# Optimization experiments

Measured on AMD Instinct MI355X. Metric: run time of the kernel, lower is better.

Reference implementation:

```python
import jax, jax.numpy as jnp
import numpy as np

B, SW, SS, D, H = 2, 1024, 256, 1024, 16  # D = hidden_dim*num_heads = 64*16


def _dense_init(key, d_in, d_out):
    # xavier_uniform kernel, zero bias
    lim = np.sqrt(6.0 / (d_in + d_out))
    k = jax.random.uniform(key, (d_in, d_out), jnp.float32, -lim, lim)
    b = jnp.zeros((d_out,), jnp.float32)
    return k, b


def setup_inputs() -> dict:
    key = jax.random.key(0)
    ks = jax.random.split(key, 16)
    inp = {
        'word_inputs': jax.random.normal(ks[0], (B, SW, D), jnp.float32),
        'word_context': jax.random.normal(ks[1], (B, SW, D), jnp.float32),
        'sentence_inputs': jax.random.normal(ks[2], (B, SS, D), jnp.float32),
        'sentence_context': jax.random.normal(ks[3], (B, SS, D), jnp.float32),
        'word_mask': jax.random.uniform(ks[4], (B, H, SW, SW), jnp.float32),
        'sentence_mask': jax.random.uniform(ks[5], (B, H, SS, SS), jnp.float32),
    }
    names = ['wq', 'wk', 'wv', 'wo', 'sq', 'sk', 'sv', 'so']
    for i, n in enumerate(names):
        kk, bb = _dense_init(ks[6 + i], D, D)
        inp[n + '_k'] = kk
        inp[n + '_b'] = bb
    return inp


def _attention(q, k, v, mask):
    # Faithful to source: split heads by raw reshape (B, H, L, hd),
    # scale by sqrt(full key dim), multiplicative mask.
    Bq, Lk, Dm = v.shape[0], v.shape[1], q.shape[-1]
    hd = Dm // H
    qh = jnp.reshape(q, (Bq, H, Lk, hd))
    kh = jnp.reshape(k, (Bq, H, Lk, hd))
    vh = jnp.reshape(v, (Bq, H, Lk, hd))
    scores = jnp.einsum('bhqd,bhkd->bhqk', qh, kh) / jnp.sqrt(jnp.float32(Dm))
    if mask is not None:
        scores = scores * mask
    attn = jax.nn.softmax(scores, axis=-1)
    ctx = jnp.einsum('bhqk,bhkd->bhqd', attn, vh)
    return attn, jnp.reshape(ctx, (Bq, Lk, Dm))


def reference(word_inputs, word_context, sentence_inputs, sentence_context,
              word_mask, sentence_mask,
              wq_k, wq_b, wk_k, wk_b, wv_k, wv_b, wo_k, wo_b,
              sq_k, sq_b, sk_k, sk_b, sv_k, sv_b, so_k, so_b):
    dense = lambda x, k, b: jnp.einsum('bld,de->ble', x, k) + b
    wq = dense(word_inputs, wq_k, wq_b)
    wk = dense(word_context, wk_k, wk_b)
    wv = dense(word_context, wv_k, wv_b)
    word_attn, word_ctx = _attention(wq, wk, wv, word_mask)
    sq = dense(sentence_inputs, sq_k, sq_b)
    sk = dense(sentence_context, sk_k, sk_b)
    sv = dense(sentence_context, sv_k, sv_b)
    sent_attn, sent_ctx = _attention(sq, sk, sv, sentence_mask)
    word_out = dense(word_ctx, wo_k, wo_b)
    sent_out = dense(sent_ctx, so_k, so_b)
    return (word_out, sent_out, word_attn, sent_attn)
```

## Files before the change

kernel.cpp:

```cpp
#include <hip/hip_runtime.h>
#include <hip/hip_bf16.h>
#include <stdint.h>

typedef __attribute__((ext_vector_type(8))) short short8;
typedef __attribute__((ext_vector_type(4))) float f32x4;

__device__ __forceinline__ f32x4 mfma16(short8 a, short8 b, f32x4 c){
  return __builtin_amdgcn_mfma_f32_16x16x32_bf16(a, b, c, 0, 0, 0);
}

union BF8 { short8 v; __hip_bfloat16 h[8]; };

__device__ __forceinline__ void gld_lds16(const void* g, void* l){
  __builtin_amdgcn_global_load_lds((const __attribute__((address_space(1))) void*)g,
                                   (__attribute__((address_space(3))) void*)l, 16, 0, 0);
}

struct GemmDesc { const __hip_bfloat16* A; const __hip_bfloat16* W; const float* bias; void* out; int M; float scale; };
struct GemmArgs { GemmDesc d[6]; };
struct PrepWArgs { const float* src[8]; };
struct CvtArgs { const float* src[4]; __hip_bfloat16* dst[4]; int n[4]; };

__global__ __launch_bounds__(256) void cvt_k(CvtArgs c){
  int z = blockIdx.z;
  int n = c.n[z];
  int i = (blockIdx.x * 256 + threadIdx.x) * 8;
  if (i >= n) return;
  const float4* s = (const float4*)(c.src[z] + i);
  float4 u0 = s[0], u1 = s[1];
  BF8 cv;
  cv.h[0] = __float2bfloat16(u0.x); cv.h[1] = __float2bfloat16(u0.y);
  cv.h[2] = __float2bfloat16(u0.z); cv.h[3] = __float2bfloat16(u0.w);
  cv.h[4] = __float2bfloat16(u1.x); cv.h[5] = __float2bfloat16(u1.y);
  cv.h[6] = __float2bfloat16(u1.z); cv.h[7] = __float2bfloat16(u1.w);
  *(short8*)(c.dst[z] + i) = cv.v;
}

__global__ __launch_bounds__(256) void prep_w_k(PrepWArgs pa, __hip_bfloat16* dst){
  __shared__ float t[64][65];
  const float* W = pa.src[blockIdx.z];
  int k0 = blockIdx.y * 64, n0 = blockIdx.x * 64;
  int c = threadIdx.x & 63, r0 = (threadIdx.x >> 6) * 16;
  #pragma unroll
  for (int i = 0; i < 16; ++i) t[r0 + i][c] = W[(size_t)(k0 + r0 + i) * 1024 + n0 + c];
  __syncthreads();
  __hip_bfloat16* D = dst + (size_t)blockIdx.z * 1048576;
  #pragma unroll
  for (int i = 0; i < 16; ++i) D[(size_t)(n0 + r0 + i) * 1024 + k0 + c] = __float2bfloat16(t[c][r0 + i]);
}

__global__ __launch_bounds__(256) void prep_v_k(const __hip_bfloat16* vw, const __hip_bfloat16* vs,
                                                __hip_bfloat16* vtw, __hip_bfloat16* vts){
  bool word = (blockIdx.z == 0);
  int L = word ? 1024 : 256;
  if (!word && blockIdx.x >= 4) return;
  __shared__ __hip_bfloat16 t[64][65];
  const __hip_bfloat16* src = (word ? vw : vs) + (size_t)blockIdx.y * L * 64;
  __hip_bfloat16* dst = (word ? vtw : vts) + (size_t)blockIdx.y * L * 64;
  int l0 = blockIdx.x * 64;
  int c = threadIdx.x & 63, r0 = (threadIdx.x >> 6) * 16;
  #pragma unroll
  for (int i = 0; i < 16; ++i) t[r0 + i][c] = src[(size_t)(l0 + r0 + i) * 64 + c];
  __syncthreads();
  #pragma unroll
  for (int i = 0; i < 16; ++i) dst[(size_t)(r0 + i) * L + l0 + c] = t[c][r0 + i];
}

template<bool OUT_BF16>
__global__ __launch_bounds__(256) void gemm_k(GemmArgs ga){
  GemmDesc dd = ga.d[blockIdx.z];
  int m0 = blockIdx.y * 128;
  if (m0 >= dd.M) return;
  int n0 = blockIdx.x * 128;

  __shared__ __align__(16) __hip_bfloat16 lA[2][128 * 32];
  __shared__ __align__(16) __hip_bfloat16 lB[2][128 * 32];

  int tid = threadIdx.x, lane = tid & 63, wv = tid >> 6;
  int r16 = lane & 15, g = lane >> 4;
  int wr = wv >> 1, wc = wv & 1;

  const __hip_bfloat16* Ab = dd.A + (size_t)m0 * 1024;
  const __hip_bfloat16* Wb = dd.W + (size_t)n0 * 1024;
  int lrow = lane >> 2;
  int scol = (lane & 3) * 8;

  #define STAGE(buf, kc)                                                            \
    {                                                                               \
      _Pragma("unroll")                                                             \
      for (int h = 0; h < 2; ++h){                                                  \
        int rbase = h * 64 + wv * 16;                                               \
        int row = rbase + lrow;                                                     \
        gld_lds16(Ab + (size_t)row * 1024 + (kc) + scol, &lA[buf][rbase * 32]);     \
        gld_lds16(Wb + (size_t)row * 1024 + (kc) + scol, &lB[buf][rbase * 32]);     \
      }                                                                             \
    }

  f32x4 acc[4][4] = {};
  STAGE(0, 0);
  int cur = 0;
  for (int kc = 0; kc < 1024; kc += 32){
    if (kc + 32 < 1024) STAGE(cur ^ 1, kc + 32);
    __syncthreads();
    const __hip_bfloat16* la = &lA[cur][(wr * 64) * 32];
    const __hip_bfloat16* lb = &lB[cur][(wc * 64) * 32];
    short8 af[4], bfr[4];
    #pragma unroll
    for (int t = 0; t < 4; ++t){
      af[t]  = *(const short8*)(la + (t * 16 + r16) * 32 + g * 8);
      bfr[t] = *(const short8*)(lb + (t * 16 + r16) * 32 + g * 8);
    }
    #pragma unroll
    for (int mt = 0; mt < 4; ++mt)
      #pragma unroll
      for (int nt = 0; nt < 4; ++nt)
        acc[mt][nt] = mfma16(af[mt], bfr[nt], acc[mt][nt]);
    __syncthreads();
    cur ^= 1;
  }
  #undef STAGE

  #pragma unroll
  for (int nt = 0; nt < 4; ++nt){
    int col = n0 + wc * 64 + nt * 16 + r16;
    float bb = dd.bias[col];
    #pragma unroll
    for (int mt = 0; mt < 4; ++mt){
      int row0 = m0 + wr * 64 + mt * 16 + g * 4;
      #pragma unroll
      for (int r = 0; r < 4; ++r){
        float v = (acc[mt][nt][r] + bb) * dd.scale;
        if (OUT_BF16) ((__hip_bfloat16*)dd.out)[(size_t)(row0 + r) * 1024 + col] = __float2bfloat16(v);
        else          ((float*)dd.out)[(size_t)(row0 + r) * 1024 + col] = v;
      }
    }
  }
}

template<int L>
__global__ __launch_bounds__(512, 6) void attn_k(
    const __hip_bfloat16* __restrict__ qb, const __hip_bfloat16* __restrict__ kb,
    const __hip_bfloat16* __restrict__ vt, const float* __restrict__ mask,
    float* __restrict__ attn, __hip_bfloat16* __restrict__ ctx){
  constexpr int KQ = L / 8, KT = KQ / 16, CH = KQ / 32;
  int bh = blockIdx.y;
  int q0 = blockIdx.x * 16;
  int lane = threadIdx.x & 63, kq = threadIdx.x >> 6;
  int r16 = lane & 15, g = lane >> 4;
  size_t ho = (size_t)bh * L * 64;
  const __hip_bfloat16* Qp = qb + ho;
  const __hip_bfloat16* Kp = kb + ho + (size_t)kq * KQ * 64;
  const __hip_bfloat16* Vp = vt + ho;
  int q = q0 + r16;
  const float* mrow = mask + (size_t)bh * L * L + (size_t)q * L + kq * KQ;
  float* arow = attn + (size_t)bh * L * L + (size_t)q * L + kq * KQ;

  short8 qf0 = *(const short8*)(Qp + (size_t)q * 64 + g * 8);
  short8 qf1 = *(const short8*)(Qp + (size_t)q * 64 + 32 + g * 8);

  f32x4 s[KT];
  #pragma unroll
  for (int kt = 0; kt < KT; ++kt){
    const __hip_bfloat16* kr = Kp + (size_t)(kt * 16 + r16) * 64 + g * 8;
    short8 kf0 = *(const short8*)kr;
    short8 kf1 = *(const short8*)(kr + 32);
    f32x4 t = {};
    t = mfma16(kf0, qf0, t);
    t = mfma16(kf1, qf1, t);
    f32x4 mv = __builtin_nontemporal_load((const f32x4*)(mrow + kt * 16 + g * 4));
    t[0] *= mv[0]; t[1] *= mv[1]; t[2] *= mv[2]; t[3] *= mv[3];
    s[kt] = t;
  }

  float mx = -3.0e38f;
  #pragma unroll
  for (int kt = 0; kt < KT; ++kt)
    #pragma unroll
    for (int r = 0; r < 4; ++r) mx = fmaxf(mx, s[kt][r]);
  mx = fmaxf(mx, __shfl_xor(mx, 16));
  mx = fmaxf(mx, __shfl_xor(mx, 32));
  __shared__ float redm[8][16], redl[8][16];
  if (lane < 16) redm[kq][lane] = mx;
  __syncthreads();
  mx = fmaxf(fmaxf(fmaxf(redm[0][r16], redm[1][r16]), fmaxf(redm[2][r16], redm[3][r16])),
             fmaxf(fmaxf(redm[4][r16], redm[5][r16]), fmaxf(redm[6][r16], redm[7][r16])));
  float sm = 0.f;
  #pragma unroll
  for (int kt = 0; kt < KT; ++kt)
    #pragma unroll
    for (int r = 0; r < 4; ++r){ float e = __expf(s[kt][r] - mx); s[kt][r] = e; sm += e; }
  sm += __shfl_xor(sm, 16);
  sm += __shfl_xor(sm, 32);
  if (lane < 16) redl[kq][lane] = sm;
  __syncthreads();
  sm = ((redl[0][r16] + redl[1][r16]) + (redl[2][r16] + redl[3][r16])) +
       ((redl[4][r16] + redl[5][r16]) + (redl[6][r16] + redl[7][r16]));
  float inv = 1.0f / sm;

  #pragma unroll
  for (int kt = 0; kt < KT; ++kt){
    f32x4 v;
    v[0] = s[kt][0] * inv; v[1] = s[kt][1] * inv;
    v[2] = s[kt][2] * inv; v[3] = s[kt][3] * inv;
    s[kt] = v;
    __builtin_nontemporal_store(v, (f32x4*)(arow + kt * 16 + g * 4));
  }

  __shared__ __align__(16) __hip_bfloat16 plds[8][16][40];
  f32x4 c4[4] = {};
  const __hip_bfloat16* vbase = Vp + kq * KQ;
  #pragma unroll
  for (int ch = 0; ch < CH; ++ch){
    #pragma unroll
    for (int t = 0; t < 2; ++t){
      union { uint64_t u; __hip_bfloat16 h[4]; } pk;
      pk.h[0] = __float2bfloat16(s[2 * ch + t][0]);
      pk.h[1] = __float2bfloat16(s[2 * ch + t][1]);
      pk.h[2] = __float2bfloat16(s[2 * ch + t][2]);
      pk.h[3] = __float2bfloat16(s[2 * ch + t][3]);
      *(uint64_t*)&plds[kq][r16][t * 16 + g * 4] = pk.u;
    }
    short8 pf = *(const short8*)&plds[kq][r16][g * 8];
    const __hip_bfloat16* vpp = vbase + ch * 32 + g * 8;
    #pragma unroll
    for (int nt = 0; nt < 4; ++nt){
      short8 vf = *(const short8*)(vpp + (size_t)(nt * 16 + r16) * L);
      c4[nt] = mfma16(pf, vf, c4[nt]);
    }
  }

  __shared__ float ctxl[8][16][65];
  #pragma unroll
  for (int nt = 0; nt < 4; ++nt)
    #pragma unroll
    for (int r = 0; r < 4; ++r) ctxl[kq][g * 4 + r][nt * 16 + r16] = c4[nt][r];
  __syncthreads();
  if (kq < 4){
    int dq = kq * 16 + g * 4;
    union { uint64_t u; __hip_bfloat16 h[4]; } ov;
    #pragma unroll
    for (int rr = 0; rr < 4; ++rr){
      float v = ((ctxl[0][r16][dq + rr] + ctxl[1][r16][dq + rr]) +
                 (ctxl[2][r16][dq + rr] + ctxl[3][r16][dq + rr])) +
                ((ctxl[4][r16][dq + rr] + ctxl[5][r16][dq + rr]) +
                 (ctxl[6][r16][dq + rr] + ctxl[7][r16][dq + rr]));
      ov.h[rr] = __float2bfloat16(v);
    }
    *(uint64_t*)(ctx + ho + (size_t)(q0 + r16) * 64 + dq) = ov.u;
  }
}

extern "C" void kernel_launch(void* const* d_in, const int* in_sizes, int n_in,
                              void* d_out, int out_size, void* d_ws, size_t ws_size,
                              hipStream_t stream){
  const float* word_mask = (const float*)d_in[4];
  const float* sent_mask = (const float*)d_in[5];

  char* ws = (char*)d_ws;
  const size_t MB = 1048576;
  __hip_bfloat16* Wt   = (__hip_bfloat16*)(ws);
  __hip_bfloat16* bwi  = (__hip_bfloat16*)(ws + 16 * MB);
  __hip_bfloat16* bwc  = (__hip_bfloat16*)(ws + 20 * MB);
  __hip_bfloat16* bsi  = (__hip_bfloat16*)(ws + 24 * MB);
  __hip_bfloat16* bsc  = (__hip_bfloat16*)(ws + 25 * MB);
  __hip_bfloat16* qw   = (__hip_bfloat16*)(ws + 26 * MB);
  __hip_bfloat16* kw   = (__hip_bfloat16*)(ws + 30 * MB);
  __hip_bfloat16* vw   = (__hip_bfloat16*)(ws + 34 * MB);
  __hip_bfloat16* sqb  = (__hip_bfloat16*)(ws + 38 * MB);
  __hip_bfloat16* skb  = (__hip_bfloat16*)(ws + 39 * MB);
  __hip_bfloat16* svb  = (__hip_bfloat16*)(ws + 40 * MB);
  __hip_bfloat16* vtw  = (__hip_bfloat16*)(ws + 41 * MB);
  __hip_bfloat16* vts  = (__hip_bfloat16*)(ws + 45 * MB);
  __hip_bfloat16* ctxw = (__hip_bfloat16*)(ws + 46 * MB);
  __hip_bfloat16* ctxs = (__hip_bfloat16*)(ws + 50 * MB);

  float* out = (float*)d_out;
  float* word_out  = out;
  float* sent_out  = out + 2097152;
  float* word_attn = out + 2621440;
  float* sent_attn = out + 36175872;

  PrepWArgs pw;
  pw.src[0] = (const float*)d_in[6];  pw.src[1] = (const float*)d_in[8];
  pw.src[2] = (const float*)d_in[10]; pw.src[3] = (const float*)d_in[12];
  pw.src[4] = (const float*)d_in[14]; pw.src[5] = (const float*)d_in[16];
  pw.src[6] = (const float*)d_in[18]; pw.src[7] = (const float*)d_in[20];
  prep_w_k<<<dim3(16, 16, 8), 256, 0, stream>>>(pw, Wt);

  CvtArgs cv;
  cv.src[0] = (const float*)d_in[0]; cv.dst[0] = bwi; cv.n[0] = 2097152;
  cv.src[1] = (const float*)d_in[1]; cv.dst[1] = bwc; cv.n[1] = 2097152;
  cv.src[2] = (const float*)d_in[2]; cv.dst[2] = bsi; cv.n[2] = 524288;
  cv.src[3] = (const float*)d_in[3]; cv.dst[3] = bsc; cv.n[3] = 524288;
  cvt_k<<<dim3(1024, 1, 4), 256, 0, stream>>>(cv);

  GemmArgs g1;
  g1.d[0] = { bwi, Wt + (size_t)0 * 1048576, (const float*)d_in[7],  qw,  2048, 1.0f / 32.0f };
  g1.d[1] = { bwc, Wt + (size_t)1 * 1048576, (const float*)d_in[9],  kw,  2048, 1.0f };
  g1.d[2] = { bwc, Wt + (size_t)2 * 1048576, (const float*)d_in[11], vw,  2048, 1.0f };
  g1.d[3] = { bsi, Wt + (size_t)4 * 1048576, (const float*)d_in[15], sqb, 512,  1.0f / 32.0f };
  g1.d[4] = { bsc, Wt + (size_t)5 * 1048576, (const float*)d_in[17], skb, 512,  1.0f };
  g1.d[5] = { bsc, Wt + (size_t)6 * 1048576, (const float*)d_in[19], svb, 512,  1.0f };
  gemm_k<true><<<dim3(8, 16, 6), 256, 0, stream>>>(g1);

  prep_v_k<<<dim3(16, 32, 2), 256, 0, stream>>>(vw, svb, vtw, vts);

  attn_k<1024><<<dim3(64, 32), 512, 0, stream>>>(qw, kw, vtw, word_mask, word_attn, ctxw);
  attn_k<256><<<dim3(16, 32), 512, 0, stream>>>(sqb, skb, vts, sent_mask, sent_attn, ctxs);

  GemmArgs g2 = {};
  g2.d[0] = { ctxw, Wt + (size_t)3 * 1048576, (const float*)d_in[13], word_out, 2048, 1.0f };
  g2.d[1] = { ctxs, Wt + (size_t)7 * 1048576, (const float*)d_in[21], sent_out, 512,  1.0f };
  gemm_k<false><<<dim3(8, 16, 2), 256, 0, stream>>>(g2);
}
```

Measured before the change: 211.0 us.

## Stage mask and attention rows through shared memory for coalesced global access

The attention kernel now first loads the block's 16 mask rows with fully coalesced row-wise f32x4 loads into a padded dynamic LDS buffer. It computes scores from that buffer and writes the normalized probabilities back into it, then stores the attention matrix to global memory row-contiguously. The PV step rereads probabilities from LDS instead of the old per-chunk bf16 staging, and the context reduction reuses the same buffer. The goal is to replace the strided 16-byte fragment accesses on the large mask and attn tensors with coalesced ones. The cost is about 64KB of LDS per block for L=1024, which lowers occupancy (launch bounds go from 6 to 4), plus extra barriers.

```diff
diff --git a/kernel.cpp b/kernel.cpp
--- a/kernel.cpp
+++ b/kernel.cpp
@@ -138,25 +138,41 @@
 }
 
 template<int L>
-__global__ __launch_bounds__(512, 6) void attn_k(
+__global__ __launch_bounds__(512, 4) void attn_k(
     const __hip_bfloat16* __restrict__ qb, const __hip_bfloat16* __restrict__ kb,
     const __hip_bfloat16* __restrict__ vt, const float* __restrict__ mask,
     float* __restrict__ attn, __hip_bfloat16* __restrict__ ctx){
   constexpr int KQ = L / 8, KT = KQ / 16, CH = KQ / 32;
+  constexpr int STR = L + 4;
+  constexpr int RQ = L / 4;
+  constexpr int SWEEPS = 16 * RQ / 512;
+  extern __shared__ __align__(16) float buf[];
+  __shared__ float redm[8][16], redl[8][16];
+
   int bh = blockIdx.y;
   int q0 = blockIdx.x * 16;
-  int lane = threadIdx.x & 63, kq = threadIdx.x >> 6;
+  int tid = threadIdx.x;
+  int lane = tid & 63, kq = tid >> 6;
   int r16 = lane & 15, g = lane >> 4;
   size_t ho = (size_t)bh * L * 64;
   const __hip_bfloat16* Qp = qb + ho;
   const __hip_bfloat16* Kp = kb + ho + (size_t)kq * KQ * 64;
   const __hip_bfloat16* Vp = vt + ho;
+  const float* mbase = mask + (size_t)bh * L * L + (size_t)q0 * L;
+  float* abase = attn + (size_t)bh * L * L + (size_t)q0 * L;
+
+  #pragma unroll
+  for (int it = 0; it < SWEEPS; ++it){
+    int f = tid + it * 512;
+    int row = f / RQ, colv = f % RQ;
+    f32x4 v = *(const f32x4*)(mbase + (size_t)row * L + colv * 4);
+    *(f32x4*)(buf + row * STR + colv * 4) = v;
+  }
+
   int q = q0 + r16;
-  const float* mrow = mask + (size_t)bh * L * L + (size_t)q * L + kq * KQ;
-  float* arow = attn + (size_t)bh * L * L + (size_t)q * L + kq * KQ;
-
   short8 qf0 = *(const short8*)(Qp + (size_t)q * 64 + g * 8);
   short8 qf1 = *(const short8*)(Qp + (size_t)q * 64 + 32 + g * 8);
+  __syncthreads();
 
   f32x4 s[KT];
   #pragma unroll
@@ -167,7 +183,7 @@
     f32x4 t = {};
     t = mfma16(kf0, qf0, t);
     t = mfma16(kf1, qf1, t);
-    f32x4 mv = __builtin_nontemporal_load((const f32x4*)(mrow + kt * 16 + g * 4));
+    f32x4 mv = *(const f32x4*)(buf + r16 * STR + kq * KQ + kt * 16 + g * 4);
     t[0] *= mv[0]; t[1] *= mv[1]; t[2] *= mv[2]; t[3] *= mv[3];
     s[kt] = t;
   }
@@ -179,7 +195,6 @@
     for (int r = 0; r < 4; ++r) mx = fmaxf(mx, s[kt][r]);
   mx = fmaxf(mx, __shfl_xor(mx, 16));
   mx = fmaxf(mx, __shfl_xor(mx, 32));
-  __shared__ float redm[8][16], redl[8][16];
   if (lane < 16) redm[kq][lane] = mx;
   __syncthreads();
   mx = fmaxf(fmaxf(fmaxf(redm[0][r16], redm[1][r16]), fmaxf(redm[2][r16], redm[3][r16])),
@@ -202,48 +217,54 @@
     f32x4 v;
     v[0] = s[kt][0] * inv; v[1] = s[kt][1] * inv;
     v[2] = s[kt][2] * inv; v[3] = s[kt][3] * inv;
-    s[kt] = v;
-    __builtin_nontemporal_store(v, (f32x4*)(arow + kt * 16 + g * 4));
-  }
-
-  __shared__ __align__(16) __hip_bfloat16 plds[8][16][40];
+    *(f32x4*)(buf + r16 * STR + kq * KQ + kt * 16 + g * 4) = v;
+  }
+  __syncthreads();
+
+  #pragma unroll
+  for (int it = 0; it < SWEEPS; ++it){
+    int f = tid + it * 512;
+    int row = f / RQ, colv = f % RQ;
+    f32x4 v = *(const f32x4*)(buf + row * STR + colv * 4);
+    *(f32x4*)(abase + (size_t)row * L + colv * 4) = v;
+  }
+
   f32x4 c4[4] = {};
   const __hip_bfloat16* vbase = Vp + kq * KQ;
   #pragma unroll
   for (int ch = 0; ch < CH; ++ch){
-    #pragma unroll
-    for (int t = 0; t < 2; ++t){
-      union { uint64_t u; __hip_bfloat16 h[4]; } pk;
-      pk.h[0] = __float2bfloat16(s[2 * ch + t][0]);
-      pk.h[1] = __float2bfloat16(s[2 * ch + t][1]);
-      pk.h[2] = __float2bfloat16(s[2 * ch + t][2]);
-      pk.h[3] = __float2bfloat16(s[2 * ch + t][3]);
-      *(uint64_t*)&plds[kq][r16][t * 16 + g * 4] = pk.u;
-    }
-    short8 pf = *(const short8*)&plds[kq][r16][g * 8];
+    const float* pp = buf + r16 * STR + kq * KQ + ch * 32 + g * 8;
+    f32x4 p0 = *(const f32x4*)pp;
+    f32x4 p1 = *(const f32x4*)(pp + 4);
+    BF8 pk;
+    pk.h[0] = __float2bfloat16(p0[0]); pk.h[1] = __float2bfloat16(p0[1]);
+    pk.h[2] = __float2bfloat16(p0[2]); pk.h[3] = __float2bfloat16(p0[3]);
+    pk.h[4] = __float2bfloat16(p1[0]); pk.h[5] = __float2bfloat16(p1[1]);
+    pk.h[6] = __float2bfloat16(p1[2]); pk.h[7] = __float2bfloat16(p1[3]);
     const __hip_bfloat16* vpp = vbase + ch * 32 + g * 8;
     #pragma unroll
     for (int nt = 0; nt < 4; ++nt){
       short8 vf = *(const short8*)(vpp + (size_t)(nt * 16 + r16) * L);
-      c4[nt] = mfma16(pf, vf, c4[nt]);
-    }
-  }
-
-  __shared__ float ctxl[8][16][65];
+      c4[nt] = mfma16(pk.v, vf, c4[nt]);
+    }
+  }
+  __syncthreads();
+
   #pragma unroll
   for (int nt = 0; nt < 4; ++nt)
     #pragma unroll
-    for (int r = 0; r < 4; ++r) ctxl[kq][g * 4 + r][nt * 16 + r16] = c4[nt][r];
+    for (int r = 0; r < 4; ++r)
+      buf[(kq * 16 + g * 4 + r) * 65 + nt * 16 + r16] = c4[nt][r];
   __syncthreads();
   if (kq < 4){
     int dq = kq * 16 + g * 4;
     union { uint64_t u; __hip_bfloat16 h[4]; } ov;
     #pragma unroll
     for (int rr = 0; rr < 4; ++rr){
-      float v = ((ctxl[0][r16][dq + rr] + ctxl[1][r16][dq + rr]) +
-                 (ctxl[2][r16][dq + rr] + ctxl[3][r16][dq + rr])) +
-                ((ctxl[4][r16][dq + rr] + ctxl[5][r16][dq + rr]) +
-                 (ctxl[6][r16][dq + rr] + ctxl[7][r16][dq + rr]));
+      float v = ((buf[(0 * 16 + r16) * 65 + dq + rr] + buf[(1 * 16 + r16) * 65 + dq + rr]) +
+                 (buf[(2 * 16 + r16) * 65 + dq + rr] + buf[(3 * 16 + r16) * 65 + dq + rr])) +
+                ((buf[(4 * 16 + r16) * 65 + dq + rr] + buf[(5 * 16 + r16) * 65 + dq + rr]) +
+                 (buf[(6 * 16 + r16) * 65 + dq + rr] + buf[(7 * 16 + r16) * 65 + dq + rr]));
       ov.h[rr] = __float2bfloat16(v);
     }
     *(uint64_t*)(ctx + ho + (size_t)(q0 + r16) * 64 + dq) = ov.u;
@@ -305,8 +326,15 @@
 
   prep_v_k<<<dim3(16, 32, 2), 256, 0, stream>>>(vw, svb, vtw, vts);
 
-  attn_k<1024><<<dim3(64, 32), 512, 0, stream>>>(qw, kw, vtw, word_mask, word_attn, ctxw);
-  attn_k<256><<<dim3(16, 32), 512, 0, stream>>>(sqb, skb, vts, sent_mask, sent_attn, ctxs);
+  const int shw = 16 * (1024 + 4) * 4;
+  const int shs = 8 * 16 * 65 * 4;
+  static int attr_done = 0;
+  (void)attr_done;
+  hipFuncSetAttribute((const void*)(void(*)(const __hip_bfloat16*, const __hip_bfloat16*,
+                                            const __hip_bfloat16*, const float*, float*, __hip_bfloat16*))attn_k<1024>,
+                      hipFuncAttributeMaxDynamicSharedMemorySize, shw);
+  attn_k<1024><<<dim3(64, 32), 512, shw, stream>>>(qw, kw, vtw, word_mask, word_attn, ctxw);
+  attn_k<256><<<dim3(16, 32), 512, shs, stream>>>(sqb, skb, vts, sent_mask, sent_attn, ctxs);
 
   GemmArgs g2 = {};
   g2.d[0] = { ctxw, Wt + (size_t)3 * 1048576, (const float*)d_in[13], word_out, 2048, 1.0f };
```

Result: faster. 186.9 us (-11.4%).

## Restructure attention PV stage to split head dim across waves via shared P

Applied to the files above, without the earlier changes.

The probability tile is now written once to a full-width shared buffer, and four waves each compute a 16-column slice of the context over the whole key length. This removes the per-wave partial context accumulators and the cross-wave reduction through shared memory. In exchange, half the waves sit idle during the PV stage and the P buffer is larger. The mask loads and attention stores also switch from nontemporal to plain memory operations.

```diff
diff --git a/kernel.cpp b/kernel.cpp
--- a/kernel.cpp
+++ b/kernel.cpp
@@ -142,18 +142,21 @@
     const __hip_bfloat16* __restrict__ qb, const __hip_bfloat16* __restrict__ kb,
     const __hip_bfloat16* __restrict__ vt, const float* __restrict__ mask,
     float* __restrict__ attn, __hip_bfloat16* __restrict__ ctx){
-  constexpr int KQ = L / 8, KT = KQ / 16, CH = KQ / 32;
+  constexpr int KQ = L / 8, KT = KQ / 16, NCH = L / 32;
+  constexpr int PSTR = L + 8;
+  __shared__ __align__(16) __hip_bfloat16 plds[16][PSTR];
+  __shared__ float redm[8][16], redl[8][16];
+
   int bh = blockIdx.y;
   int q0 = blockIdx.x * 16;
-  int lane = threadIdx.x & 63, kq = threadIdx.x >> 6;
+  int lane = threadIdx.x & 63, wv = threadIdx.x >> 6;
   int r16 = lane & 15, g = lane >> 4;
   size_t ho = (size_t)bh * L * 64;
   const __hip_bfloat16* Qp = qb + ho;
-  const __hip_bfloat16* Kp = kb + ho + (size_t)kq * KQ * 64;
-  const __hip_bfloat16* Vp = vt + ho;
+  const __hip_bfloat16* Kp = kb + ho + (size_t)wv * KQ * 64;
   int q = q0 + r16;
-  const float* mrow = mask + (size_t)bh * L * L + (size_t)q * L + kq * KQ;
-  float* arow = attn + (size_t)bh * L * L + (size_t)q * L + kq * KQ;
+  const float* mrow = mask + (size_t)bh * L * L + (size_t)q * L + wv * KQ;
+  float* arow = attn + (size_t)bh * L * L + (size_t)q * L + wv * KQ;
 
   short8 qf0 = *(const short8*)(Qp + (size_t)q * 64 + g * 8);
   short8 qf1 = *(const short8*)(Qp + (size_t)q * 64 + 32 + g * 8);
@@ -167,7 +170,7 @@
     f32x4 t = {};
     t = mfma16(kf0, qf0, t);
     t = mfma16(kf1, qf1, t);
-    f32x4 mv = __builtin_nontemporal_load((const f32x4*)(mrow + kt * 16 + g * 4));
+    f32x4 mv = *(const f32x4*)(mrow + kt * 16 + g * 4);
     t[0] *= mv[0]; t[1] *= mv[1]; t[2] *= mv[2]; t[3] *= mv[3];
     s[kt] = t;
   }
@@ -179,8 +182,7 @@
     for (int r = 0; r < 4; ++r) mx = fmaxf(mx, s[kt][r]);
   mx = fmaxf(mx, __shfl_xor(mx, 16));
   mx = fmaxf(mx, __shfl_xor(mx, 32));
-  __shared__ float redm[8][16], redl[8][16];
-  if (lane < 16) redm[kq][lane] = mx;
+  if (lane < 16) redm[wv][lane] = mx;
   __syncthreads();
   mx = fmaxf(fmaxf(fmaxf(redm[0][r16], redm[1][r16]), fmaxf(redm[2][r16], redm[3][r16])),
              fmaxf(fmaxf(redm[4][r16], redm[5][r16]), fmaxf(redm[6][r16], redm[7][r16])));
@@ -191,7 +193,7 @@
     for (int r = 0; r < 4; ++r){ float e = __expf(s[kt][r] - mx); s[kt][r] = e; sm += e; }
   sm += __shfl_xor(sm, 16);
   sm += __shfl_xor(sm, 32);
-  if (lane < 16) redl[kq][lane] = sm;
+  if (lane < 16) redl[wv][lane] = sm;
   __syncthreads();
   sm = ((redl[0][r16] + redl[1][r16]) + (redl[2][r16] + redl[3][r16])) +
        ((redl[4][r16] + redl[5][r16]) + (redl[6][r16] + redl[7][r16]));
@@ -202,51 +204,26 @@
     f32x4 v;
     v[0] = s[kt][0] * inv; v[1] = s[kt][1] * inv;
     v[2] = s[kt][2] * inv; v[3] = s[kt][3] * inv;
-    s[kt] = v;
-    __builtin_nontemporal_store(v, (f32x4*)(arow + kt * 16 + g * 4));
-  }
-
-  __shared__ __align__(16) __hip_bfloat16 plds[8][16][40];
-  f32x4 c4[4] = {};
-  const __hip_bfloat16* vbase = Vp + kq * KQ;
-  #pragma unroll
-  for (int ch = 0; ch < CH; ++ch){
-    #pragma unroll
-    for (int t = 0; t < 2; ++t){
-      union { uint64_t u; __hip_bfloat16 h[4]; } pk;
-      pk.h[0] = __float2bfloat16(s[2 * ch + t][0]);
-      pk.h[1] = __float2bfloat16(s[2 * ch + t][1]);
-      pk.h[2] = __float2bfloat16(s[2 * ch + t][2]);
-      pk.h[3] = __float2bfloat16(s[2 * ch + t][3]);
-      *(uint64_t*)&plds[kq][r16][t * 16 + g * 4] = pk.u;
-    }
-    short8 pf = *(const short8*)&plds[kq][r16][g * 8];
-    const __hip_bfloat16* vpp = vbase + ch * 32 + g * 8;
-    #pragma unroll
-    for (int nt = 0; nt < 4; ++nt){
-      short8 vf = *(const short8*)(vpp + (size_t)(nt * 16 + r16) * L);
-      c4[nt] = mfma16(pf, vf, c4[nt]);
-    }
-  }
-
-  __shared__ float ctxl[8][16][65];
-  #pragma unroll
-  for (int nt = 0; nt < 4; ++nt)
-    #pragma unroll
-    for (int r = 0; r < 4; ++r) ctxl[kq][g * 4 + r][nt * 16 + r16] = c4[nt][r];
-  __syncthreads();
-  if (kq < 4){
-    int dq = kq * 16 + g * 4;
-    union { uint64_t u; __hip_bfloat16 h[4]; } ov;
-    #pragma unroll
-    for (int rr = 0; rr < 4; ++rr){
-      float v = ((ctxl[0][r16][dq + rr] + ctxl[1][r16][dq + rr]) +
-                 (ctxl[2][r16][dq + rr] + ctxl[3][r16][dq + rr])) +
-                ((ctxl[4][r16][dq + rr] + ctxl[5][r16][dq + rr]) +
-                 (ctxl[6][r16][dq + rr] + ctxl[7][r16][dq + rr]));
-      ov.h[rr] = __float2bfloat16(v);
-    }
-    *(uint64_t*)(ctx + ho + (size_t)(q0 + r16) * 64 + dq) = ov.u;
+    *(f32x4*)(arow + kt * 16 + g * 4) = v;
+    union { uint64_t u; __hip_bfloat16 h[4]; } pk;
+    pk.h[0] = __float2bfloat16(v[0]); pk.h[1] = __float2bfloat16(v[1]);
+    pk.h[2] = __float2bfloat16(v[2]); pk.h[3] = __float2bfloat16(v[3]);
+    *(uint64_t*)&plds[r16][wv * KQ + kt * 16 + g * 4] = pk.u;
+  }
+  __syncthreads();
+
+  if (wv < 4){
+    const __hip_bfloat16* vb = vt + ho + (size_t)(wv * 16 + r16) * L;
+    f32x4 c = {};
+    #pragma unroll
+    for (int ch = 0; ch < NCH; ++ch){
+      short8 pf = *(const short8*)&plds[r16][ch * 32 + g * 8];
+      short8 vf = *(const short8*)(vb + ch * 32 + g * 8);
+      c = mfma16(pf, vf, c);
+    }
+    #pragma unroll
+    for (int r = 0; r < 4; ++r)
+      ctx[ho + (size_t)(q0 + g * 4 + r) * 64 + wv * 16 + r16] = __float2bfloat16(c[r]);
   }
 }
 
```

Measured after the change: 212.3 us. About the same (+0.6%).
